# Optimization experiments

Hardware: AMD Instinct MI355X
Metric: run time of the kernel (lower is better)

## Reference

```python
import jax, jax.numpy as jnp
import numpy as np

N_NODES = 100000
N_EDGES = 640000
WIDTH = 128
LAYERS = 3
N_GRAPHS = 64


def setup_inputs() -> dict:
    key = jax.random.key(0)
    ks = jax.random.split(key, 6)
    x = jax.random.normal(ks[0], (N_NODES, WIDTH), dtype=jnp.float32)
    edge_index = jax.random.randint(ks[1], (2, N_EDGES), 0, N_NODES, dtype=jnp.int64)
    edge_attr = jax.random.uniform(ks[2], (N_EDGES, 1), dtype=jnp.float32)
    batch = jnp.sort(jax.random.randint(ks[3], (N_NODES,), 0, N_GRAPHS, dtype=jnp.int64))
    Ws = jax.random.normal(ks[4], (LAYERS, WIDTH, WIDTH), dtype=jnp.float32) / np.sqrt(WIDTH)
    bs = jnp.zeros((LAYERS, WIDTH), dtype=jnp.float32)
    return {"x": x, "edge_index": edge_index, "edge_attr": edge_attr,
            "batch": batch, "Ws": Ws, "bs": bs}


def reference(x, edge_index, edge_attr, batch, Ws, bs):
    N = x.shape[0]
    ew = edge_attr.squeeze()  # [E]
    loop = jnp.arange(N)
    # add self-loops with fill_value=2.0 (improved=True)
    row = jnp.concatenate([edge_index[0], loop])
    col = jnp.concatenate([edge_index[1], loop])
    w = jnp.concatenate([ew, jnp.full((N,), 2.0, dtype=ew.dtype)])
    # symmetric gcn normalization: deg computed at target (col)
    deg = jax.ops.segment_sum(w, col, num_segments=N)
    dinv = jnp.where(deg > 0, jax.lax.rsqrt(deg), 0.0)
    norm = dinv[row] * w * dinv[col]  # [E+N]

    for l in range(LAYERS):
        h = x @ Ws[l]  # [N, WIDTH]
        msg = norm[:, None] * h[row]  # gather + scale
        x = jax.ops.segment_sum(msg, col, num_segments=N) + bs[l]

    # global mean pool over graphs
    sums = jax.ops.segment_sum(x, batch, num_segments=N_GRAPHS)
    counts = jax.ops.segment_sum(jnp.ones((N,), dtype=x.dtype), batch, num_segments=N_GRAPHS)
    return sums / jnp.maximum(counts, 1.0)[:, None]
```

## Files before the change

kernel.cpp:

```cpp
#include <hip/hip_runtime.h>
#include <hip/hip_fp16.h>
#include <cstddef>

#define N_NODES  100000
#define N_EDGES  640000
#define WIDTH    128
#define LAYERS   3
#define N_GRAPHS 64
#define ELL_K    40

#define GLOAD_LDS16(gsrc, ldst) \
  __builtin_amdgcn_global_load_lds( \
      (const __attribute__((address_space(1))) unsigned*)(gsrc), \
      (__attribute__((address_space(3))) unsigned*)(ldst), 16, 0, 0)

__device__ __forceinline__ float h2f(unsigned short h) {
  __half x; *reinterpret_cast<unsigned short*>(&x) = h;
  return __half2float(x);
}
__device__ __forceinline__ unsigned short f2h(float f) {
  __half h = __float2half_rn(f);
  return *reinterpret_cast<unsigned short*>(&h);
}


__global__ void k_init(int* __restrict__ cursor, float* __restrict__ deg) {
  int i = blockIdx.x * blockDim.x + threadIdx.x;
  if (i < N_NODES) { cursor[i] = 0; deg[i] = 0.f; }
}

__global__ void k_fill_cd(const int* __restrict__ row, const int* __restrict__ col,
                          const float* __restrict__ ew,
                          int* __restrict__ cursor, float* __restrict__ deg,
                          int2* __restrict__ ell) {
  int e = blockIdx.x * blockDim.x + threadIdx.x;
  if (e < N_EDGES) {
    int r = row[e], c = col[e];
    float w = ew[e];
    atomicAdd(&deg[c], w);
    int slot = atomicAdd(&cursor[r], 1);
    if (slot < ELL_K) {
      int2 pk; pk.x = c; pk.y = __float_as_int(w);
      ell[(size_t)r * ELL_K + slot] = pk;
    }
  }
}

__global__ void k_dinv_e(const float* __restrict__ deg, float* __restrict__ dinv,
                         float* __restrict__ d2, float* __restrict__ sq) {
  int v = blockIdx.x * blockDim.x + threadIdx.x;
  if (v < N_NODES) {
    float d = 2.0f + deg[v];
    float di = (d > 0.0f) ? 1.0f / sqrtf(d) : 0.0f;
    dinv[v] = di;
    d2[v] = di * di;
    sq[v] = sqrtf(d);
  }
}

__device__ __forceinline__ int lbound(const int* __restrict__ batch, int key) {
  int lo = 0, hi = N_NODES;
  while (lo < hi) { int m = (lo + hi) >> 1; if (batch[m] < key) lo = m + 1; else hi = m; }
  return lo;
}

__global__ void k_cntg(const int* __restrict__ batch, int* __restrict__ cntg,
                       float* __restrict__ invc) {
  int g = threadIdx.x;
  if (g < N_GRAPHS) {
    int lb = lbound(batch, g), ub = lbound(batch, g + 1);
    int c = ub - lb;
    cntg[g] = c;
    invc[g] = 1.0f / (float)max(c, 1);
  }
}

__global__ void k_pinit(const int* __restrict__ batch, const float* __restrict__ invc,
                        const float* __restrict__ dinv, unsigned short* __restrict__ p) {
  const int total = N_NODES * 16;
  for (int i = blockIdx.x * blockDim.x + threadIdx.x; i < total;
       i += gridDim.x * blockDim.x) {
    int v = i >> 4, q = i & 15;
    int b = batch[v];
    unsigned short val = f2h(invc[b] * dinv[v]);
    ushort4 u;
    ((unsigned short*)&u)[0] = (q * 4 + 0 == b) ? val : (unsigned short)0;
    ((unsigned short*)&u)[1] = (q * 4 + 1 == b) ? val : (unsigned short)0;
    ((unsigned short*)&u)[2] = (q * 4 + 2 == b) ? val : (unsigned short)0;
    ((unsigned short*)&u)[3] = (q * 4 + 3 == b) ? val : (unsigned short)0;
    ((ushort4*)p)[i] = u;
  }
}

#define CS_BLOCKS 512
__global__ __launch_bounds__(256) void k_colsum(
    const unsigned short* __restrict__ y, const float* __restrict__ sq,
    float* __restrict__ partc) {
  __shared__ float4 sd[256];
  int t = threadIdx.x;
  int slot = t & 15;
  int vrow = t >> 4;
  const int chunk = (N_NODES + CS_BLOCKS - 1) / CS_BLOCKS;
  int start = blockIdx.x * chunk;
  int end = min(start + chunk, N_NODES);
  float4 acc = {0.f, 0.f, 0.f, 0.f};
  for (int v = start + vrow; v < end; v += 16) {
    ushort4 u = ((const ushort4*)(y + (size_t)v * 64))[slot];
    float rd = sq[v];
    acc.x += h2f(u.x) * rd; acc.y += h2f(u.y) * rd;
    acc.z += h2f(u.z) * rd; acc.w += h2f(u.w) * rd;
  }
  sd[t] = acc;
  __syncthreads();
  for (int off = 8; off > 0; off >>= 1) {
    if (vrow < off) {
      float4 o = sd[(vrow + off) * 16 + slot];
      acc.x += o.x; acc.y += o.y; acc.z += o.z; acc.w += o.w;
      sd[t] = acc;
    }
    __syncthreads();
  }
  if (vrow == 0)
    ((float4*)(partc + (size_t)blockIdx.x * 64))[slot] = acc;
}

__global__ __launch_bounds__(256) void k_cs2(
    const float* __restrict__ csA, const float* __restrict__ csB,
    float* __restrict__ ps, float* __restrict__ pas) {
  __shared__ float sd[256];
  const float* src = (blockIdx.x == 0) ? csA : csB;
  float* dst = (blockIdx.x == 0) ? ps : pas;
  int t = threadIdx.x;
  int g = t & 63, c = t >> 6;
  float a = 0.f;
  for (int r = c * 128; r < (c + 1) * 128; r++) a += src[r * 64 + g];
  sd[t] = a;
  __syncthreads();
  if (t < 128) sd[t] += sd[t + 128];
  __syncthreads();
  if (t < 64) dst[t] = sd[t] + sd[t + 64];
}

#define AGG_NPB 4
__global__ __launch_bounds__(256) void k_yagg(
    const unsigned short* __restrict__ yin, const int* __restrict__ cnt_a,
    const int2* __restrict__ ell, const float* __restrict__ scale,
    unsigned short* __restrict__ yout) {
  int wave = threadIdx.x >> 6;
  int lane = threadIdx.x & 63;
  int v = blockIdx.x * AGG_NPB + wave;
  if (v >= N_NODES) return;
  int vv = __builtin_amdgcn_readfirstlane(v);
  int grp = lane >> 4;
  int q = lane & 15;

  ushort4 hvu = ((const ushort4*)(yin + (size_t)vv * 64))[q];
  int cnt = cnt_a[vv];

  float4 a0 = {0,0,0,0}, a1 = {0,0,0,0}, a2 = {0,0,0,0}, a3 = {0,0,0,0};
  int2 pk = (lane < cnt) ? ell[(size_t)vv * ELL_K + lane] : make_int2(0, 0);
  int   si = pk.x;
  float swv = __int_as_float(pk.y);

  for (int base = 0; base < cnt; base += 16) {
    int e0 = base + grp;
    float w0 = __shfl(swv, e0); int i0 = __shfl(si, e0);
    ushort4 u0 = ((const ushort4*)(yin + (size_t)i0 * 64))[q];
    a0.x += w0 * h2f(u0.x); a0.y += w0 * h2f(u0.y);
    a0.z += w0 * h2f(u0.z); a0.w += w0 * h2f(u0.w);
    if (base + 4 < cnt) {
      int e1 = base + 4 + grp;
      float w1 = __shfl(swv, e1); int i1 = __shfl(si, e1);
      ushort4 u1 = ((const ushort4*)(yin + (size_t)i1 * 64))[q];
      a1.x += w1 * h2f(u1.x); a1.y += w1 * h2f(u1.y);
      a1.z += w1 * h2f(u1.z); a1.w += w1 * h2f(u1.w);
    }
    if (base + 8 < cnt) {
      int e2 = base + 8 + grp;
      int e3 = base + 12 + grp;
      float w2 = __shfl(swv, e2); int i2 = __shfl(si, e2);
      float w3 = __shfl(swv, e3); int i3 = __shfl(si, e3);
      ushort4 u2 = ((const ushort4*)(yin + (size_t)i2 * 64))[q];
      ushort4 u3 = ((const ushort4*)(yin + (size_t)i3 * 64))[q];
      a2.x += w2 * h2f(u2.x); a2.y += w2 * h2f(u2.y);
      a2.z += w2 * h2f(u2.z); a2.w += w2 * h2f(u2.w);
      a3.x += w3 * h2f(u3.x); a3.y += w3 * h2f(u3.y);
      a3.z += w3 * h2f(u3.z); a3.w += w3 * h2f(u3.w);
    }
  }

  a0.x += a1.x + a2.x + a3.x;
  a0.y += a1.y + a2.y + a3.y;
  a0.z += a1.z + a2.z + a3.z;
  a0.w += a1.w + a2.w + a3.w;
#pragma unroll
  for (int d = 16; d <= 32; d <<= 1) {
    a0.x += __shfl_xor(a0.x, d);
    a0.y += __shfl_xor(a0.y, d);
    a0.z += __shfl_xor(a0.z, d);
    a0.w += __shfl_xor(a0.w, d);
  }

  if (grp == 0) {
    float sc = scale[vv];
    ushort4 r;
    r.x = f2h(sc * (a0.x + 2.0f * h2f(hvu.x)));
    r.y = f2h(sc * (a0.y + 2.0f * h2f(hvu.y)));
    r.z = f2h(sc * (a0.z + 2.0f * h2f(hvu.z)));
    r.w = f2h(sc * (a0.w + 2.0f * h2f(hvu.w)));
    ((ushort4*)(yout + (size_t)vv * 64))[q] = r;
  }
}

#define CT_BLOCKS 768
#define CT_NCHUNK ((N_NODES + 63) / 64)

__global__ __launch_bounds__(256) void k_contract(
    const float* __restrict__ x0, const unsigned short* __restrict__ y3,
    float* __restrict__ part) {
  __shared__ __align__(16) float xs[64 * 128];
  __shared__ __align__(16) float ysf[64 * 64];
  int t = threadIdx.x;
  int w = t >> 6;
  int lane = t & 63;
  int j = lane * 2;

  float2 acc[16];
#pragma unroll
  for (int i = 0; i < 16; i++) acc[i] = make_float2(0.f, 0.f);

  for (int c = blockIdx.x; c < CT_NCHUNK; c += gridDim.x) {
    int cc = min(64, N_NODES - c * 64);
    int bx = cc * 512;
    int byh = cc * 128;
    const char* gx = (const char*)(x0 + (size_t)c * 64 * 128);
    const char* gy = (const char*)(y3 + (size_t)c * 64 * 64);
    __syncthreads();
#pragma unroll
    for (int i = 0; i < 8; i++) {
      int off = i * 4096 + t * 16;
      if (off < bx) GLOAD_LDS16(gx + off, (char*)xs + off);
    }
    ushort4 u[4];
#pragma unroll
    for (int r = 0; r < 4; r++) {
      int off = (r * 256 + t) * 8;
      u[r] = (off < byh) ? *(const ushort4*)(gy + off)
                         : make_ushort4(0, 0, 0, 0);
    }
#pragma unroll
    for (int r = 0; r < 4; r++) {
      int idx = (r * 256 + t) * 4;
      if (idx < cc * 64)
        *(float4*)(ysf + idx) = make_float4(h2f(u[r].x), h2f(u[r].y),
                                            h2f(u[r].z), h2f(u[r].w));
    }
    asm volatile("s_waitcnt vmcnt(0)" ::: "memory");
    __syncthreads();

    int v = 0;
    for (; v + 2 <= cc; v += 2) {
      float2 xa = *(const float2*)(xs + v * 128 + j);
      float2 xb = *(const float2*)(xs + (v + 1) * 128 + j);
      const float4* ya = (const float4*)(ysf + v * 64 + w * 16);
      const float4* yb = (const float4*)(ysf + (v + 1) * 64 + w * 16);
      float4 a0 = ya[0], a1 = ya[1], a2 = ya[2], a3 = ya[3];
      float4 b0 = yb[0], b1 = yb[1], b2 = yb[2], b3 = yb[3];
      float yas[16] = {a0.x, a0.y, a0.z, a0.w, a1.x, a1.y, a1.z, a1.w,
                       a2.x, a2.y, a2.z, a2.w, a3.x, a3.y, a3.z, a3.w};
      float ybs[16] = {b0.x, b0.y, b0.z, b0.w, b1.x, b1.y, b1.z, b1.w,
                       b2.x, b2.y, b2.z, b2.w, b3.x, b3.y, b3.z, b3.w};
#pragma unroll
      for (int i = 0; i < 16; i++) {
        acc[i].x += yas[i] * xa.x;
        acc[i].y += yas[i] * xa.y;
      }
#pragma unroll
      for (int i = 0; i < 16; i++) {
        acc[i].x += ybs[i] * xb.x;
        acc[i].y += ybs[i] * xb.y;
      }
    }
    if (v < cc) {
      float2 xa = *(const float2*)(xs + v * 128 + j);
      const float4* ya = (const float4*)(ysf + v * 64 + w * 16);
      float4 a0 = ya[0], a1 = ya[1], a2 = ya[2], a3 = ya[3];
      float yas[16] = {a0.x, a0.y, a0.z, a0.w, a1.x, a1.y, a1.z, a1.w,
                       a2.x, a2.y, a2.z, a2.w, a3.x, a3.y, a3.z, a3.w};
#pragma unroll
      for (int i = 0; i < 16; i++) {
        acc[i].x += yas[i] * xa.x;
        acc[i].y += yas[i] * xa.y;
      }
    }
  }

  float* dst = part + (size_t)blockIdx.x * (N_GRAPHS * WIDTH);
#pragma unroll
  for (int i = 0; i < 16; i++)
    *(float2*)(dst + (w * 16 + i) * WIDTH + j) = acc[i];
}

#define RC_ROWS 64
#define RC_RG (CT_BLOCKS / RC_ROWS)

__global__ __launch_bounds__(256) void k_reduce1(
    const float* __restrict__ part, float* __restrict__ part2) {
  int bid = blockIdx.x, t = threadIdx.x;
  int rg = bid >> 5, colc = bid & 31;
  int idx = colc * 256 + t;
  const float* src = part + (size_t)rg * RC_ROWS * (N_GRAPHS * WIDTH) + idx;
  float a0 = 0.f, a1 = 0.f, a2 = 0.f, a3 = 0.f;
  for (int r = 0; r < RC_ROWS; r += 4) {
    a0 += src[(size_t)(r + 0) * (N_GRAPHS * WIDTH)];
    a1 += src[(size_t)(r + 1) * (N_GRAPHS * WIDTH)];
    a2 += src[(size_t)(r + 2) * (N_GRAPHS * WIDTH)];
    a3 += src[(size_t)(r + 3) * (N_GRAPHS * WIDTH)];
  }
  part2[rg * (N_GRAPHS * WIDTH) + idx] = (a0 + a1) + (a2 + a3);
}

__global__ __launch_bounds__(WIDTH) void k_mm128(
    const float* __restrict__ A, const float* __restrict__ B, float* __restrict__ O) {
  __shared__ float Ar[WIDTH];
  int r = blockIdx.x, j = threadIdx.x;
  Ar[j] = A[r * WIDTH + j];
  __syncthreads();
  float a = 0.f;
#pragma unroll 8
  for (int k = 0; k < WIDTH; k++) a += Ar[k] * B[k * WIDTH + j];
  O[r * WIDTH + j] = a;
}

__global__ __launch_bounds__(WIDTH) void k_c01(
    const float* __restrict__ b0, const float* __restrict__ T1,
    const float* __restrict__ b1, const float* __restrict__ W2,
    float* __restrict__ c0, float* __restrict__ c1) {
  __shared__ float s0[WIDTH], s1v[WIDTH];
  int j = threadIdx.x;
  s0[j] = b0[j]; s1v[j] = b1[j];
  __syncthreads();
  float a0 = 0.f, a1 = 0.f;
#pragma unroll 8
  for (int k = 0; k < WIDTH; k++) {
    a0 += s0[k] * T1[k * WIDTH + j];
    a1 += s1v[k] * W2[k * WIDTH + j];
  }
  c0[j] = a0; c1[j] = a1;
}

__global__ __launch_bounds__(WIDTH) void k_out(
    const float* __restrict__ part2, const float* __restrict__ Wp,
    const float* __restrict__ c0, const float* __restrict__ c1,
    const float* __restrict__ ps, const float* __restrict__ pas,
    const int* __restrict__ cntg, const float* __restrict__ b2,
    float* __restrict__ out) {
  __shared__ float Cr[WIDTH];
  int g = blockIdx.x, j = threadIdx.x;
  float cv = 0.f;
#pragma unroll
  for (int rg = 0; rg < RC_RG; rg++)
    cv += part2[rg * (N_GRAPHS * WIDTH) + g * WIDTH + j];
  Cr[j] = cv;
  __syncthreads();
  float a = pas[g] * c0[j] + ps[g] * c1[j] + ((cntg[g] > 0) ? b2[j] : 0.f);
#pragma unroll 8
  for (int k = 0; k < WIDTH; k++) a += Cr[k] * Wp[k * WIDTH + j];
  out[g * WIDTH + j] = a;
}


extern "C" void kernel_launch(void* const* d_in, const int* in_sizes, int n_in,
                              void* d_out, int out_size, void* d_ws, size_t ws_size,
                              hipStream_t stream) {
  const float* x   = (const float*)d_in[0];
  const int* row   = (const int*)d_in[1];
  const int* col   = row + N_EDGES;
  const float* ew  = (const float*)d_in[2];
  const int* batch = (const int*)d_in[3];
  const float* Ws  = (const float*)d_in[4];
  const float* bs  = (const float*)d_in[5];
  float* out = (float*)d_out;

  char* w = (char*)d_ws;
  float* dinv    = (float*)(w + 0);
  float* d2      = (float*)(w + 400128);
  float* sq      = (float*)(w + 800256);
  float* deg     = (float*)(w + 1200384);
  int*   cursor  = (int*)(w + 1600512);
  int*   cntg    = (int*)(w + 2000640);
  float* invc    = (float*)(w + 2000896);
  float* ps      = (float*)(w + 2001152);
  float* pas     = (float*)(w + 2001408);
  float* T1      = (float*)(w + 2001664);
  float* Wp      = (float*)(w + 2067200);
  float* c0      = (float*)(w + 2132736);
  float* c1      = (float*)(w + 2133248);
  int2*  ell     = (int2*)(w + 2133760);
  float* part    = (float*)(w + 34133760);
  float* part2   = (float*)(w + 67688192);
  unsigned short* yA = (unsigned short*)(w + 68212480);
  unsigned short* yB = (unsigned short*)(w + 81012480);
  float* csA     = (float*)(w + 93812480);
  float* csB     = (float*)(w + 93943552);

  int nb_n = (N_NODES + 255) / 256;
  int nb_e = (N_EDGES + 255) / 256;

  k_init   <<<nb_n, 256, 0, stream>>>(cursor, deg);
  k_fill_cd<<<nb_e, 256, 0, stream>>>(row, col, ew, cursor, deg, ell);
  k_dinv_e <<<nb_n, 256, 0, stream>>>(deg, dinv, d2, sq);

  k_cntg <<<1, 64, 0, stream>>>(batch, cntg, invc);
  k_pinit<<<2048, 256, 0, stream>>>(batch, invc, dinv, yA);

  int nb_y = (N_NODES + AGG_NPB - 1) / AGG_NPB;
  k_yagg  <<<nb_y, 256, 0, stream>>>(yA, cursor, ell, d2, yB);
  k_colsum<<<CS_BLOCKS, 256, 0, stream>>>(yB, sq, csA);
  k_yagg  <<<nb_y, 256, 0, stream>>>(yB, cursor, ell, d2, yA);
  k_colsum<<<CS_BLOCKS, 256, 0, stream>>>(yA, sq, csB);
  k_yagg  <<<nb_y, 256, 0, stream>>>(yA, cursor, ell, dinv, yB);

  k_cs2  <<<2, 256, 0, stream>>>(csA, csB, ps, pas);
  k_mm128<<<WIDTH, WIDTH, 0, stream>>>(Ws + 1 * WIDTH * WIDTH, Ws + 2 * WIDTH * WIDTH, T1);
  k_mm128<<<WIDTH, WIDTH, 0, stream>>>(Ws + 0 * WIDTH * WIDTH, T1, Wp);
  k_c01  <<<1, WIDTH, 0, stream>>>(bs, T1, bs + WIDTH, Ws + 2 * WIDTH * WIDTH, c0, c1);

  k_contract<<<CT_BLOCKS, 256, 0, stream>>>(x, yB, part);
  k_reduce1 <<<RC_RG * 32, 256, 0, stream>>>(part, part2);
  k_out     <<<N_GRAPHS, WIDTH, 0, stream>>>(part2, Wp, c0, c1, ps, pas, cntg,
                                             bs + 2 * WIDTH, out);
}
```

Measured before the change: 274.1 us.

## Fuse column-sum into aggregation kernel and process four nodes per wave

Drops the separate column-sum kernels and folds the sq-weighted column sum into the aggregation epilogue. Each block writes a per-block partial that k_cs2 then reduces over YBLK rows. Each wave now handles four consecutive nodes, with their ELL entries and self features loaded up front for more memory-level parallelism. The cost is two fewer launches and less re-reading of y. In exchange the grid shrinks fourfold, register pressure rises, and a larger partial buffer must be reduced serially by the two-block k_cs2.

After: 605.3 us. 121% more time.

```diff
diff --git a/kernel.cpp b/kernel.cpp
--- a/kernel.cpp
+++ b/kernel.cpp
@@ -8,6 +8,8 @@
 #define LAYERS   3
 #define N_GRAPHS 64
 #define ELL_K    40
+#define YN       4
+#define YBLK     (N_NODES / 16)
 
 #define GLOAD_LDS16(gsrc, ldst) \
   __builtin_amdgcn_global_load_lds( \
@@ -92,38 +94,6 @@
   }
 }
 
-#define CS_BLOCKS 512
-__global__ __launch_bounds__(256) void k_colsum(
-    const unsigned short* __restrict__ y, const float* __restrict__ sq,
-    float* __restrict__ partc) {
-  __shared__ float4 sd[256];
-  int t = threadIdx.x;
-  int slot = t & 15;
-  int vrow = t >> 4;
-  const int chunk = (N_NODES + CS_BLOCKS - 1) / CS_BLOCKS;
-  int start = blockIdx.x * chunk;
-  int end = min(start + chunk, N_NODES);
-  float4 acc = {0.f, 0.f, 0.f, 0.f};
-  for (int v = start + vrow; v < end; v += 16) {
-    ushort4 u = ((const ushort4*)(y + (size_t)v * 64))[slot];
-    float rd = sq[v];
-    acc.x += h2f(u.x) * rd; acc.y += h2f(u.y) * rd;
-    acc.z += h2f(u.z) * rd; acc.w += h2f(u.w) * rd;
-  }
-  sd[t] = acc;
-  __syncthreads();
-  for (int off = 8; off > 0; off >>= 1) {
-    if (vrow < off) {
-      float4 o = sd[(vrow + off) * 16 + slot];
-      acc.x += o.x; acc.y += o.y; acc.z += o.z; acc.w += o.w;
-      sd[t] = acc;
-    }
-    __syncthreads();
-  }
-  if (vrow == 0)
-    ((float4*)(partc + (size_t)blockIdx.x * 64))[slot] = acc;
-}
-
 __global__ __launch_bounds__(256) void k_cs2(
     const float* __restrict__ csA, const float* __restrict__ csB,
     float* __restrict__ ps, float* __restrict__ pas) {
@@ -133,7 +103,7 @@
   int t = threadIdx.x;
   int g = t & 63, c = t >> 6;
   float a = 0.f;
-  for (int r = c * 128; r < (c + 1) * 128; r++) a += src[r * 64 + g];
+  for (int r = c; r < YBLK; r += 4) a += src[(size_t)r * 64 + g];
   sd[t] = a;
   __syncthreads();
   if (t < 128) sd[t] += sd[t + 128];
@@ -141,74 +111,104 @@
   if (t < 64) dst[t] = sd[t] + sd[t + 64];
 }
 
-#define AGG_NPB 4
 __global__ __launch_bounds__(256) void k_yagg(
     const unsigned short* __restrict__ yin, const int* __restrict__ cnt_a,
     const int2* __restrict__ ell, const float* __restrict__ scale,
-    unsigned short* __restrict__ yout) {
+    const float* __restrict__ sq, unsigned short* __restrict__ yout,
+    float* __restrict__ partc) {
+  __shared__ float4 sdc[4][16];
   int wave = threadIdx.x >> 6;
   int lane = threadIdx.x & 63;
-  int v = blockIdx.x * AGG_NPB + wave;
-  if (v >= N_NODES) return;
-  int vv = __builtin_amdgcn_readfirstlane(v);
+  int base = (blockIdx.x * 4 + wave) * YN;
   int grp = lane >> 4;
   int q = lane & 15;
 
-  ushort4 hvu = ((const ushort4*)(yin + (size_t)vv * 64))[q];
-  int cnt = cnt_a[vv];
-
-  float4 a0 = {0,0,0,0}, a1 = {0,0,0,0}, a2 = {0,0,0,0}, a3 = {0,0,0,0};
-  int2 pk = (lane < cnt) ? ell[(size_t)vv * ELL_K + lane] : make_int2(0, 0);
-  int   si = pk.x;
-  float swv = __int_as_float(pk.y);
-
-  for (int base = 0; base < cnt; base += 16) {
-    int e0 = base + grp;
-    float w0 = __shfl(swv, e0); int i0 = __shfl(si, e0);
-    ushort4 u0 = ((const ushort4*)(yin + (size_t)i0 * 64))[q];
-    a0.x += w0 * h2f(u0.x); a0.y += w0 * h2f(u0.y);
-    a0.z += w0 * h2f(u0.z); a0.w += w0 * h2f(u0.w);
-    if (base + 4 < cnt) {
-      int e1 = base + 4 + grp;
-      float w1 = __shfl(swv, e1); int i1 = __shfl(si, e1);
-      ushort4 u1 = ((const ushort4*)(yin + (size_t)i1 * 64))[q];
-      a1.x += w1 * h2f(u1.x); a1.y += w1 * h2f(u1.y);
-      a1.z += w1 * h2f(u1.z); a1.w += w1 * h2f(u1.w);
-    }
-    if (base + 8 < cnt) {
-      int e2 = base + 8 + grp;
-      int e3 = base + 12 + grp;
-      float w2 = __shfl(swv, e2); int i2 = __shfl(si, e2);
-      float w3 = __shfl(swv, e3); int i3 = __shfl(si, e3);
-      ushort4 u2 = ((const ushort4*)(yin + (size_t)i2 * 64))[q];
-      ushort4 u3 = ((const ushort4*)(yin + (size_t)i3 * 64))[q];
-      a2.x += w2 * h2f(u2.x); a2.y += w2 * h2f(u2.y);
-      a2.z += w2 * h2f(u2.z); a2.w += w2 * h2f(u2.w);
-      a3.x += w3 * h2f(u3.x); a3.y += w3 * h2f(u3.y);
-      a3.z += w3 * h2f(u3.z); a3.w += w3 * h2f(u3.w);
-    }
-  }
-
-  a0.x += a1.x + a2.x + a3.x;
-  a0.y += a1.y + a2.y + a3.y;
-  a0.z += a1.z + a2.z + a3.z;
-  a0.w += a1.w + a2.w + a3.w;
-#pragma unroll
-  for (int d = 16; d <= 32; d <<= 1) {
-    a0.x += __shfl_xor(a0.x, d);
-    a0.y += __shfl_xor(a0.y, d);
-    a0.z += __shfl_xor(a0.z, d);
-    a0.w += __shfl_xor(a0.w, d);
-  }
-
-  if (grp == 0) {
-    float sc = scale[vv];
-    ushort4 r;
-    r.x = f2h(sc * (a0.x + 2.0f * h2f(hvu.x)));
-    r.y = f2h(sc * (a0.y + 2.0f * h2f(hvu.y)));
-    r.z = f2h(sc * (a0.z + 2.0f * h2f(hvu.z)));
-    r.w = f2h(sc * (a0.w + 2.0f * h2f(hvu.w)));
-    ((ushort4*)(yout + (size_t)vv * 64))[q] = r;
+  int cnt[YN]; int2 pk[YN]; ushort4 hvu[YN];
+#pragma unroll
+  for (int i = 0; i < YN; i++) {
+    int v = base + i;
+    cnt[i] = cnt_a[v];
+    pk[i] = (lane < cnt[i]) ? ell[(size_t)v * ELL_K + lane] : make_int2(0, 0);
+    hvu[i] = ((const ushort4*)(yin + (size_t)v * 64))[q];
+  }
+
+  float4 cs = {0.f, 0.f, 0.f, 0.f};
+#pragma unroll
+  for (int i = 0; i < YN; i++) {
+    int v = base + i;
+    int cn = cnt[i];
+    int si = pk[i].x;
+    float swv = __int_as_float(pk[i].y);
+    float4 a0 = {0,0,0,0}, a1 = {0,0,0,0}, a2 = {0,0,0,0}, a3 = {0,0,0,0};
+
+    for (int b = 0; b < cn; b += 16) {
+      int e0 = b + grp;
+      float w0 = __shfl(swv, e0); int i0 = __shfl(si, e0);
+      ushort4 u0 = ((const ushort4*)(yin + (size_t)i0 * 64))[q];
+      a0.x += w0 * h2f(u0.x); a0.y += w0 * h2f(u0.y);
+      a0.z += w0 * h2f(u0.z); a0.w += w0 * h2f(u0.w);
+      if (b + 4 < cn) {
+        int e1 = b + 4 + grp;
+        float w1 = __shfl(swv, e1); int i1 = __shfl(si, e1);
+        ushort4 u1 = ((const ushort4*)(yin + (size_t)i1 * 64))[q];
+        a1.x += w1 * h2f(u1.x); a1.y += w1 * h2f(u1.y);
+        a1.z += w1 * h2f(u1.z); a1.w += w1 * h2f(u1.w);
+      }
+      if (b + 8 < cn) {
+        int e2 = b + 8 + grp;
+        int e3 = b + 12 + grp;
+        float w2 = __shfl(swv, e2); int i2 = __shfl(si, e2);
+        float w3 = __shfl(swv, e3); int i3 = __shfl(si, e3);
+        ushort4 u2 = ((const ushort4*)(yin + (size_t)i2 * 64))[q];
+        ushort4 u3 = ((const ushort4*)(yin + (size_t)i3 * 64))[q];
+        a2.x += w2 * h2f(u2.x); a2.y += w2 * h2f(u2.y);
+        a2.z += w2 * h2f(u2.z); a2.w += w2 * h2f(u2.w);
+        a3.x += w3 * h2f(u3.x); a3.y += w3 * h2f(u3.y);
+        a3.z += w3 * h2f(u3.z); a3.w += w3 * h2f(u3.w);
+      }
+    }
+
+    a0.x += a1.x + a2.x + a3.x;
+    a0.y += a1.y + a2.y + a3.y;
+    a0.z += a1.z + a2.z + a3.z;
+    a0.w += a1.w + a2.w + a3.w;
+#pragma unroll
+    for (int d = 16; d <= 32; d <<= 1) {
+      a0.x += __shfl_xor(a0.x, d);
+      a0.y += __shfl_xor(a0.y, d);
+      a0.z += __shfl_xor(a0.z, d);
+      a0.w += __shfl_xor(a0.w, d);
+    }
+
+    if (grp == 0) {
+      float sc = scale[v];
+      float rx = sc * (a0.x + 2.0f * h2f(hvu[i].x));
+      float ry = sc * (a0.y + 2.0f * h2f(hvu[i].y));
+      float rz = sc * (a0.z + 2.0f * h2f(hvu[i].z));
+      float rw = sc * (a0.w + 2.0f * h2f(hvu[i].w));
+      ushort4 r;
+      r.x = f2h(rx); r.y = f2h(ry); r.z = f2h(rz); r.w = f2h(rw);
+      ((ushort4*)(yout + (size_t)v * 64))[q] = r;
+      if (partc) {
+        float wv = sq[v];
+        cs.x += wv * rx; cs.y += wv * ry;
+        cs.z += wv * rz; cs.w += wv * rw;
+      }
+    }
+  }
+
+  if (partc) {
+    if (grp == 0) sdc[wave][q] = cs;
+    __syncthreads();
+    if (threadIdx.x < 16) {
+      int qq = threadIdx.x;
+      float4 a = sdc[0][qq], b = sdc[1][qq], c = sdc[2][qq], d = sdc[3][qq];
+      a.x += b.x + c.x + d.x;
+      a.y += b.y + c.y + d.y;
+      a.z += b.z + c.z + d.z;
+      a.w += b.w + c.w + d.w;
+      ((float4*)(partc + (size_t)blockIdx.x * 64))[qq] = a;
+    }
   }
 }
 
@@ -402,7 +402,7 @@
   unsigned short* yA = (unsigned short*)(w + 68212480);
   unsigned short* yB = (unsigned short*)(w + 81012480);
   float* csA     = (float*)(w + 93812480);
-  float* csB     = (float*)(w + 93943552);
+  float* csB     = (float*)(w + 95412480);
 
   int nb_n = (N_NODES + 255) / 256;
   int nb_e = (N_EDGES + 255) / 256;
@@ -414,12 +414,9 @@
   k_cntg <<<1, 64, 0, stream>>>(batch, cntg, invc);
   k_pinit<<<2048, 256, 0, stream>>>(batch, invc, dinv, yA);
 
-  int nb_y = (N_NODES + AGG_NPB - 1) / AGG_NPB;
-  k_yagg  <<<nb_y, 256, 0, stream>>>(yA, cursor, ell, d2, yB);
-  k_colsum<<<CS_BLOCKS, 256, 0, stream>>>(yB, sq, csA);
-  k_yagg  <<<nb_y, 256, 0, stream>>>(yB, cursor, ell, d2, yA);
-  k_colsum<<<CS_BLOCKS, 256, 0, stream>>>(yA, sq, csB);
-  k_yagg  <<<nb_y, 256, 0, stream>>>(yA, cursor, ell, dinv, yB);
+  k_yagg<<<YBLK, 256, 0, stream>>>(yA, cursor, ell, d2, sq, yB, csA);
+  k_yagg<<<YBLK, 256, 0, stream>>>(yB, cursor, ell, d2, sq, yA, csB);
+  k_yagg<<<YBLK, 256, 0, stream>>>(yA, cursor, ell, dinv, sq, yB, nullptr);
 
   k_cs2  <<<2, 256, 0, stream>>>(csA, csB, ps, pas);
   k_mm128<<<WIDTH, WIDTH, 0, stream>>>(Ws + 1 * WIDTH * WIDTH, Ws + 2 * WIDTH * WIDTH, T1);
```
